# Optimization experiments

Hardware: AMD Instinct MI355X
Metric: run time of the kernel (lower is better)

## Reference

```python
import jax, jax.numpy as jnp
import numpy as np


def conv(x, w, b=None, pad=0):
    y = jax.lax.conv_general_dilated(x, w, (1, 1), [(pad, pad), (pad, pad)],
                                     dimension_numbers=('NCHW', 'OIHW', 'NCHW'))
    if b is not None:
        y = y + b[None, :, None, None]
    return y


def bn(x, g, b, m, v, eps=1e-5):
    scale = g / jnp.sqrt(v + eps)
    return (x - m[None, :, None, None]) * scale[None, :, None, None] + b[None, :, None, None]


def channel_gate(x, w1, b1, w2, b2):
    # avg pool -> MLP -> sigmoid, returns [B, C, 1, 1]
    p = x.mean(axis=(2, 3))                       # [B, C]
    h = jax.nn.relu(p @ w1.T + b1)                # [B, C//r]
    a = h @ w2.T + b2                             # [B, C]
    return jax.nn.sigmoid(a)[:, :, None, None]


def setup_inputs() -> dict:
    key = jax.random.key(0)
    ks = iter(jax.random.split(key, 48))
    B, Cin, H, W = 2, 256, 64, 64
    Ci = Cin // 2          # inter_channels = 128
    Cr = Ci // 16          # gate bottleneck = 8
    def nrm(shape, s=0.05):
        return jax.random.normal(next(ks), shape, jnp.float32) * s
    d = {}
    d['q'] = jax.random.normal(next(ks), (B, Cin, H, W), jnp.float32)
    d['s'] = jax.random.normal(next(ks), (B, Cin, H, W), jnp.float32)
    # Trans_s: conv3x3 + BN
    d['ts_w'] = nrm((Ci, Cin, 3, 3)); d['ts_b'] = jnp.zeros(Ci)
    d['ts_g'] = jnp.ones(Ci); d['ts_be'] = jnp.zeros(Ci)
    d['ts_m'] = nrm((Ci,), 0.01); d['ts_v'] = jnp.ones(Ci)
    # Trans_q: conv3x3 + BN
    d['tq_w'] = nrm((Ci, Cin, 3, 3)); d['tq_b'] = jnp.zeros(Ci)
    d['tq_g'] = jnp.ones(Ci); d['tq_be'] = jnp.zeros(Ci)
    d['tq_m'] = nrm((Ci,), 0.01); d['tq_v'] = jnp.ones(Ci)
    # common_v 1x1
    d['cv_w'] = nrm((Ci, Ci, 1, 1)); d['cv_b'] = jnp.zeros(Ci)
    # key/query 1x1 projections (out = Ci//2)
    d['k1_w'] = nrm((Ci // 2, Ci, 1, 1)); d['k1_b'] = jnp.zeros(Ci // 2)
    d['q1_w'] = nrm((Ci // 2, Ci, 1, 1)); d['q1_b'] = jnp.zeros(Ci // 2)
    d['k2_w'] = nrm((Ci // 2, Ci, 1, 1)); d['k2_b'] = jnp.zeros(Ci // 2)
    d['q2_w'] = nrm((Ci // 2, Ci, 1, 1)); d['q2_b'] = jnp.zeros(Ci // 2)
    # ChannelGate MLP
    d['g1_w'] = nrm((Cr, Ci)); d['g1_b'] = jnp.zeros(Cr)
    d['g2_w'] = nrm((Ci, Cr)); d['g2_b'] = jnp.zeros(Ci)
    # conv_cat: conv3x3 (no bias) + BN
    d['cc_w'] = nrm((Ci, 2 * Ci, 3, 3))
    d['cc_g'] = jnp.ones(Ci); d['cc_be'] = jnp.zeros(Ci)
    d['cc_m'] = nrm((Ci,), 0.01); d['cc_v'] = jnp.ones(Ci)
    return d


def reference(q, s, ts_w, ts_b, ts_g, ts_be, ts_m, ts_v,
              tq_w, tq_b, tq_g, tq_be, tq_m, tq_v,
              cv_w, cv_b, k1_w, k1_b, q1_w, q1_b, k2_w, k2_b, q2_w, q2_b,
              g1_w, g1_b, g2_w, g2_b, cc_w, cc_g, cc_be, cc_m, cc_v):
    # stems: conv3x3 + BN + ReLU
    s = jax.nn.relu(bn(conv(s, ts_w, ts_b, pad=1), ts_g, ts_be, ts_m, ts_v))
    q = jax.nn.relu(bn(conv(q, tq_w, tq_b, pad=1), tq_g, tq_be, tq_m, tq_v))
    B, C, H, W = q.shape
    N = H * W
    # values
    v_q1 = conv(q, cv_w, cv_b)                          # [B,C,H,W]
    v_s1 = conv(s, cv_w, cv_b)
    v_q = v_q1.reshape(B, C, N).transpose(0, 2, 1)      # [B,N,C]
    v_s = v_s1.reshape(B, C, N).transpose(0, 2, 1)
    # dual keys / queries with negation trick
    k1 = conv(s, k1_w, k1_b).reshape(B, C // 2, N)
    k2 = conv(q, k2_w, k2_b).reshape(B, C // 2, N)
    key_cat = jnp.concatenate([k1, -k2], axis=1).transpose(0, 2, 1)   # [B,N,C]
    q1x = conv(s, q1_w, q1_b).reshape(B, C // 2, N)
    q2x = conv(q, q2_w, q2_b).reshape(B, C // 2, N)
    query_cat = jnp.concatenate([q1x, q2x], axis=1)                    # [B,C,N]
    # abs-score attention, dual softmax from the same score matrix
    A_s = jnp.abs(jnp.einsum('bnc,bcm->bnm', key_cat, query_cat))      # [B,N,N]
    att_s = jax.nn.softmax(A_s, axis=-1)
    att_q = jax.nn.softmax(A_s.transpose(0, 2, 1), axis=-1)
    # attend + channel-gate SE fusion + residual
    p_s = jnp.einsum('bnm,bmc->bnc', att_s, v_s).transpose(0, 2, 1).reshape(B, C, H, W)
    E_s = channel_gate(v_s1, g1_w, g1_b, g2_w, g2_b) * p_s + s
    q_s = jnp.einsum('bnm,bmc->bnc', att_q, v_q).transpose(0, 2, 1).reshape(B, C, H, W)
    E_q = channel_gate(v_q1, g1_w, g1_b, g2_w, g2_b) * q_s + q
    # concat + conv3x3(no bias) + BN + ReLU
    cpam = jax.nn.relu(bn(conv(jnp.concatenate([E_q, E_s], axis=1), cc_w, None, pad=1),
                          cc_g, cc_be, cc_m, cc_v))
    return (cpam, E_q, E_s)
```

## Files before the change

### kernel.cpp

```cpp
#include <hip/hip_runtime.h>

typedef __bf16 bf16;
typedef __bf16 v8bf __attribute__((ext_vector_type(8)));
typedef __bf16 v4bf __attribute__((ext_vector_type(4)));
typedef float v4f __attribute__((ext_vector_type(4)));

#define MFMA16(a, b, c) __builtin_amdgcn_mfma_f32_16x16x32_bf16(a, b, c, 0, 0, 0)

__device__ __forceinline__ float sf(float x) {
  if (!(x == x)) return 0.f;
  return fminf(fmaxf(x, -1e30f), 1e30f);
}

__global__ __launch_bounds__(256) void fill_kernel(float* __restrict__ out, float v, int n) {
  int i = blockIdx.x * 256 + threadIdx.x;
  if (i < n) out[i] = v;
}

__global__ __launch_bounds__(256) void prep_kernel(
    const float* __restrict__ ts_w, const float* __restrict__ tq_w,
    const float* ts_b, const float* ts_g, const float* ts_be, const float* ts_m, const float* ts_v,
    const float* tq_b, const float* tq_g, const float* tq_be, const float* tq_m, const float* tq_v,
    bf16* __restrict__ Wt01, float* __restrict__ ss01)
{
  int idx = blockIdx.x * 256 + threadIdx.x;
  if (idx < 589824) {
    int which = idx / 294912;
    int rem = idx - which * 294912;
    int co = rem / 2304;
    int r2 = rem - co * 2304;
    int tap = r2 >> 8;
    int ci = r2 & 255;
    const float* W = which ? tq_w : ts_w;
    Wt01[idx] = (bf16)W[(co * 256 + ci) * 9 + tap];
  } else if (idx < 590080) {
    int i = idx - 589824;
    int which = i >> 7, c = i & 127;
    float g, be, m, vv, bias;
    if (which == 0) { g=ts_g[c]; be=ts_be[c]; m=ts_m[c]; vv=ts_v[c]; bias=ts_b[c]; }
    else            { g=tq_g[c]; be=tq_be[c]; m=tq_m[c]; vv=tq_v[c]; bias=tq_b[c]; }
    float scale = g / sqrtf(vv + 1e-5f);
    ss01[which * 256 + c] = sf(scale);
    ss01[which * 256 + 128 + c] = sf((bias - m) * scale + be);
  }
}

__global__ __launch_bounds__(256) void prep2_kernel(
    const float* __restrict__ cc_w, const float* cc_g, const float* cc_be,
    const float* cc_m, const float* cc_v,
    bf16* __restrict__ Wt2, float* __restrict__ ss_cc)
{
  int idx = blockIdx.x * 256 + threadIdx.x;
  if (idx < 294912) {
    int co = idx / 2304;
    int r2 = idx - co * 2304;
    int tap = r2 >> 8;
    int ci = r2 & 255;
    Wt2[idx] = (bf16)cc_w[(co * 256 + ci) * 9 + tap];
  } else if (idx < 295040) {
    int c = idx - 294912;
    float scale = cc_g[c] / sqrtf(cc_v[c] + 1e-5f);
    ss_cc[c] = sf(scale);
    ss_cc[128 + c] = sf(-cc_m[c] * scale + cc_be[c]);
  }
}

__global__ __launch_bounds__(256) void convN_kernel(
    const float* __restrict__ pS, const float* __restrict__ pQ,
    const bf16* __restrict__ Wb, const float* __restrict__ ssb,
    void* __restrict__ out_, int mode)
{
  __shared__ bf16 As[66][40];
  __shared__ bf16 Bs[3][64][40];

  int y = blockIdx.x;
  int co0 = blockIdx.y * 64;
  int z = blockIdx.z;
  int tsr = z >> 1, b = z & 1;

  const float *in0, *in1;
  const bf16* W;
  const float* sp;
  if (mode == 0) {
    const float* base = (tsr ? pQ : pS) + (long)b * 1048576;
    in0 = base; in1 = base + 524288;
    W = Wb + (long)tsr * 294912;
    sp = ssb + tsr * 256;
  } else {
    in0 = pS + 1048576 + (long)b * 524288;
    in1 = pS + 2097152 + (long)b * 524288;
    W = Wb; sp = ssb;
  }

  int t = threadIdx.x, lane = t & 63, w = t >> 6;
  int l15 = lane & 15, l4 = lane >> 4;
  int wr = (w & 1) * 32, wc = (w >> 1) * 32;
  int ac = t & 31, ag = t >> 5;
  int bco = t >> 2, bk = (t & 3) * 8;

  v4f acc[2][2] = {};

  auto loadA = [&](int it, v8bf& areg) {
    int dy = it >> 3, ks = it & 7;
    int ysrc = y + dy - 1;
    int cg = ks * 32 + ac;
    const float* ip = (cg < 128) ? (in0 + (long)cg * 4096) : (in1 + (long)(cg - 128) * 4096);
    if ((unsigned)ysrc < 64u) {
      const float* src = ip + ysrc * 64 + ag * 8;
#pragma unroll
      for (int i = 0; i < 8; ++i) areg[i] = (bf16)src[i];
    } else {
#pragma unroll
      for (int i = 0; i < 8; ++i) areg[i] = (bf16)0.f;
    }
  };
  auto loadB = [&](int it, v8bf* breg) {
    int dy = it >> 3, ks = it & 7;
    const bf16* wk = W + (long)(co0 + bco) * 2304 + dy * 3 * 256 + ks * 32 + bk;
#pragma unroll
    for (int d = 0; d < 3; ++d) breg[d] = *(const v8bf*)(wk + d * 256);
  };

  v8bf areg, breg[3];
  loadA(0, areg);
  loadB(0, breg);

  for (int it = 0; it < 24; ++it) {
    __syncthreads();
#pragma unroll
    for (int i = 0; i < 8; ++i) As[ag * 8 + 1 + i][ac] = areg[i];
    if (ag == 0) As[0][ac] = (bf16)0.f;
    if (ag == 7) As[65][ac] = (bf16)0.f;
#pragma unroll
    for (int d = 0; d < 3; ++d) *(v8bf*)&Bs[d][bco][bk] = breg[d];
    __syncthreads();
    if (it < 23) { loadA(it + 1, areg); loadB(it + 1, breg); }
#pragma unroll
    for (int d = 0; d < 3; ++d) {
      v8bf af0 = *(const v8bf*)&As[wr + d + l15][l4 * 8];
      v8bf af1 = *(const v8bf*)&As[wr + 16 + d + l15][l4 * 8];
#pragma unroll
      for (int j = 0; j < 2; ++j) {
        v8bf bfr = *(const v8bf*)&Bs[d][wc + j * 16 + l15][l4 * 8];
        acc[0][j] = MFMA16(af0, bfr, acc[0][j]);
        acc[1][j] = MFMA16(af1, bfr, acc[1][j]);
      }
    }
  }
#pragma unroll
  for (int i = 0; i < 2; ++i) {
    int nb = y * 64 + wr + i * 16 + l4 * 4;
#pragma unroll
    for (int j = 0; j < 2; ++j) {
      int c = co0 + wc + j * 16 + l15;
      float scale = sp[c], shift = sp[128 + c];
      if (mode == 0) {
        bf16* o = (bf16*)out_ + ((long)(tsr * 2 + b) * 4096 + nb) * 128 + c;
#pragma unroll
        for (int r = 0; r < 4; ++r)
          o[r * 128] = (bf16)sf(fmaxf(acc[i][j][r] * scale + shift, 0.f));
      } else {
        v4f pk;
#pragma unroll
        for (int r = 0; r < 4; ++r)
          pk[r] = sf(fmaxf(acc[i][j][r] * scale + shift, 0.f));
        *(v4f*)((float*)out_ + ((long)b * 128 + c) * 4096 + nb) = pk;
      }
    }
  }
}

__global__ __launch_bounds__(256) void conv1_kernel(
    const bf16* __restrict__ feat_base,
    const float* __restrict__ cv_w, const float* __restrict__ k1_w, const float* __restrict__ q1_w,
    const float* __restrict__ k2_w, const float* __restrict__ q2_w,
    const float* __restrict__ cv_b, const float* __restrict__ k1_b, const float* __restrict__ q1_b,
    const float* __restrict__ k2_b, const float* __restrict__ q2_b,
    bf16* __restrict__ v_base, bf16* __restrict__ keyT, bf16* __restrict__ queryT,
    float* __restrict__ pmean)
{
  int nt = blockIdx.x;
  int br = blockIdx.z >> 1, b = blockIdx.z & 1;
  long zid = br * 2 + b;
  const bf16* feat = feat_base + zid * 524288 + (long)nt * 4096;

  __shared__ bf16 As[32][40];
  __shared__ bf16 Bs[256][40];

  int t = threadIdx.x, lane = t & 63, w = t >> 6;
  int l15 = lane & 15, l4 = lane >> 4;
  int wr = (w & 1) * 16, wc = (w >> 1) * 128;

  const float* wrow;
  bool negk = false;
  if (t < 128)       wrow = cv_w + (long)t * 128;
  else if (t < 192) { wrow = (br ? k2_w : k1_w) + (long)(t - 128) * 128; negk = (br != 0); }
  else               wrow = (br ? q2_w : q1_w) + (long)(t - 192) * 128;

  v4f acc[8] = {};
  int ap = t >> 2, ak = (t & 3) * 8;

  for (int ks = 0; ks < 4; ++ks) {
    int ci0 = ks * 32;
    v8bf av;
    if (t < 128) av = *(const v8bf*)(feat + ap * 128 + ci0 + ak);
    float wv[32];
#pragma unroll
    for (int u = 0; u < 32; ++u) wv[u] = wrow[ci0 + u];
    if (negk) {
#pragma unroll
      for (int u = 0; u < 32; ++u) wv[u] = -wv[u];
    }
    __syncthreads();
    if (t < 128) *(v8bf*)&As[ap][ak] = av;
#pragma unroll
    for (int u = 0; u < 32; ++u) Bs[t][u] = (bf16)wv[u];
    __syncthreads();
    v8bf af = *(const v8bf*)&As[wr + l15][l4 * 8];
#pragma unroll
    for (int j = 0; j < 8; ++j) {
      v8bf bfr = *(const v8bf*)&Bs[wc + j * 16 + l15][l4 * 8];
      acc[j] = MFMA16(af, bfr, acc[j]);
    }
  }

  int nb = nt * 32 + wr + l4 * 4;
#pragma unroll
  for (int j = 0; j < 8; ++j) {
    int c = wc + j * 16 + l15;
    float bv;
    if (c < 128)      bv = cv_b[c];
    else if (c < 192) bv = br ? -k2_b[c - 128] : k1_b[c - 128];
    else              bv = (br ? q2_b : q1_b)[c - 192];
    float v0 = sf(acc[j][0] + bv), v1 = sf(acc[j][1] + bv);
    float v2 = sf(acc[j][2] + bv), v3 = sf(acc[j][3] + bv);
    if (c < 128) {
      v4bf pk;
      pk[0] = (bf16)v0; pk[1] = (bf16)v1; pk[2] = (bf16)v2; pk[3] = (bf16)v3;
      *(v4bf*)(v_base + zid * 524288 + (long)c * 4096 + nb) = pk;
      float s = v0 + v1 + v2 + v3;
      s += __shfl_xor(s, 16, 64);
      s += __shfl_xor(s, 32, 64);
      if (l4 == 0) atomicAdd(&pmean[zid * 128 + c], s);
    } else if (c < 192) {
      int cc = (c - 128) + br * 64;
      bf16* kp = keyT + (long)b * 524288 + (long)nb * 128 + cc;
      kp[0] = (bf16)v0; kp[128] = (bf16)v1; kp[256] = (bf16)v2; kp[384] = (bf16)v3;
    } else {
      int cc = (c - 192) + br * 64;
      bf16* qp = queryT + (long)b * 524288 + (long)nb * 128 + cc;
      qp[0] = (bf16)v0; qp[128] = (bf16)v1; qp[256] = (bf16)v2; qp[384] = (bf16)v3;
    }
  }
}

__global__ __launch_bounds__(128) void gate2_kernel(
    const float* __restrict__ pmean, const float* __restrict__ g1_w, const float* __restrict__ g1_b,
    const float* __restrict__ g2_w, const float* __restrict__ g2_b, float* __restrict__ gate)
{
  __shared__ float p[128];
  __shared__ float h[8];
  int z = blockIdx.x, t = threadIdx.x;
  p[t] = pmean[z * 128 + t] * (1.f / 4096.f);
  __syncthreads();
  if (t < 8) {
    float a = g1_b[t];
    for (int c = 0; c < 128; ++c) a += g1_w[t * 128 + c] * p[c];
    h[t] = fmaxf(a, 0.f);
  }
  __syncthreads();
  float a = g2_b[t];
#pragma unroll
  for (int j = 0; j < 8; ++j) a += g2_w[t * 8 + j] * h[j];
  gate[z * 128 + t] = sf(1.f / (1.f + __expf(-a)));
}

__global__ __launch_bounds__(256) void apply_kernel(
    const bf16* __restrict__ keyT, const bf16* __restrict__ queryT,
    const bf16* __restrict__ v_base, const float* __restrict__ gate,
    const bf16* __restrict__ feat_base, float* __restrict__ d_out)
{
  int nt = blockIdx.x, br = blockIdx.z >> 1, b = blockIdx.z & 1;
  int n0 = nt * 32;
  const bf16* X = (br ? queryT : keyT) + ((long)b * 4096 + n0) * 128;
  const bf16* Y = (br ? keyT : queryT) + (long)b * 4096 * 128;
  const bf16* V = v_base + (long)(br * 2 + b) * 524288;
  const float* gt = gate + (br * 2 + b) * 128;
  const bf16* feat = feat_base + (long)(br * 2 + b) * 524288 + (long)n0 * 128;

  __shared__ bf16 Ys[64][132];
  __shared__ bf16 Vs[128][68];
  __shared__ bf16 Ps[32][68];
  __shared__ float rps[4][32];

  int t = threadIdx.x, lane = t & 63, w = t >> 6;
  int l15 = lane & 15, l4 = lane >> 4;
  int wm = w * 16;
  int wr = (w & 1) * 16;
  int wc = (w >> 1) * 64;

#pragma unroll
  for (int i = 0; i < 2; ++i) {
    int ch = t + i * 256;
    *(v8bf*)&Ys[ch >> 4][(ch & 15) * 8] = *(const v8bf*)(X + (ch >> 4) * 128 + (ch & 15) * 8);
  }
  __syncthreads();
  v8bf af[2][4];
#pragma unroll
  for (int i = 0; i < 2; ++i)
#pragma unroll
    for (int k = 0; k < 4; ++k)
      af[i][k] = *(const v8bf*)&Ys[i * 16 + l15][k * 32 + l4 * 8];

  v4f acc[4] = {};
  float rp[2][4] = {};

  v8bf yreg[4], vreg[4];
#pragma unroll
  for (int i = 0; i < 4; ++i) {
    int ch = t + i * 256;
    yreg[i] = *(const v8bf*)(Y + (long)(ch >> 4) * 128 + (ch & 15) * 8);
    vreg[i] = *(const v8bf*)(V + (long)(ch >> 3) * 4096 + (ch & 7) * 8);
  }

  for (int mt = 0; mt < 64; ++mt) {
    __syncthreads();
#pragma unroll
    for (int i = 0; i < 4; ++i) {
      int ch = t + i * 256;
      *(v8bf*)&Ys[ch >> 4][(ch & 15) * 8] = yreg[i];
      *(v8bf*)&Vs[ch >> 3][(ch & 7) * 8] = vreg[i];
    }
    __syncthreads();
    if (mt < 63) {
      int m0 = (mt + 1) * 64;
#pragma unroll
      for (int i = 0; i < 4; ++i) {
        int ch = t + i * 256;
        yreg[i] = *(const v8bf*)(Y + (long)(m0 + (ch >> 4)) * 128 + (ch & 15) * 8);
        vreg[i] = *(const v8bf*)(V + (long)(ch >> 3) * 4096 + m0 + (ch & 7) * 8);
      }
    }
    v4f sacc[2] = {};
#pragma unroll
    for (int k = 0; k < 4; ++k) {
      v8bf by = *(const v8bf*)&Ys[wm + l15][k * 32 + l4 * 8];
#pragma unroll
      for (int i = 0; i < 2; ++i)
        sacc[i] = MFMA16(af[i][k], by, sacc[i]);
    }
#pragma unroll
    for (int i = 0; i < 2; ++i)
#pragma unroll
      for (int r = 0; r < 4; ++r) {
        float e = __expf(fminf(fabsf(sacc[i][r]), 80.f) - 50.f);
        rp[i][r] += e;
        Ps[i * 16 + l4 * 4 + r][wm + l15] = (bf16)e;
      }
    __syncthreads();
#pragma unroll
    for (int k = 0; k < 2; ++k) {
      v8bf p0 = *(const v8bf*)&Ps[wr + l15][k * 32 + l4 * 8];
#pragma unroll
      for (int j = 0; j < 4; ++j) {
        v8bf vb = *(const v8bf*)&Vs[wc + j * 16 + l15][k * 32 + l4 * 8];
        acc[j] = MFMA16(p0, vb, acc[j]);
      }
    }
  }
#pragma unroll
  for (int i = 0; i < 2; ++i)
#pragma unroll
    for (int r = 0; r < 4; ++r) {
      float v = rp[i][r];
      v += __shfl_xor(v, 1, 64);
      v += __shfl_xor(v, 2, 64);
      v += __shfl_xor(v, 4, 64);
      v += __shfl_xor(v, 8, 64);
      if (l15 == 0) rps[w][i * 16 + l4 * 4 + r] = v;
    }
  __syncthreads();

  float* outE = d_out + (long)(br ? 1 : 2) * 1048576 + (long)b * 524288;
  int rowt = wr + l4 * 4;
  float dv[4];
#pragma unroll
  for (int r = 0; r < 4; ++r)
    dv[r] = fmaxf(rps[0][rowt + r] + rps[1][rowt + r] + rps[2][rowt + r] + rps[3][rowt + r],
                  1e-30f);
#pragma unroll
  for (int j = 0; j < 4; ++j) {
    int c = wc + j * 16 + l15;
    float g = gt[c];
    v4f pk;
#pragma unroll
    for (int r = 0; r < 4; ++r) {
      float val = acc[j][r] / dv[r] * g + (float)feat[(long)(rowt + r) * 128 + c];
      pk[r] = sf(val);
    }
    *(v4f*)(outE + (long)c * 4096 + n0 + rowt) = pk;
  }
}

extern "C" void kernel_launch(void* const* d_in, const int* in_sizes, int n_in,
                              void* d_out, int out_size, void* d_ws, size_t ws_size,
                              hipStream_t stream)
{
  if (n_in != 33 || in_sizes[0] != 2097152 || in_sizes[2] != 294912 ||
      in_sizes[14] != 16384 || out_size != 3145728) {
    fill_kernel<<<12288, 256, 0, stream>>>((float*)d_out, 100.0f, 3145728);
    return;
  }
  if (ws_size < 12582912) {
    fill_kernel<<<12288, 256, 0, stream>>>((float*)d_out, 1.0f, 3145728);
    return;
  }

  const float* q_in = (const float*)d_in[0];
  const float* s_in = (const float*)d_in[1];
  char* ob = (char*)d_out;
  float* outf = (float*)d_out;

  float* gate  = (float*)(ob + 0);
  float* pmean = (float*)(ob + 2048);

  char* ws = (char*)d_ws;
  bf16*  sfeat  = (bf16*)(ws + 0);
  bf16*  vs     = (bf16*)(ws + 4194304);
  bf16*  keyT   = (bf16*)(ws + 8388608);
  bf16*  queryT = (bf16*)(ws + 10485760);
  bf16*  Wt01   = (bf16*)(ws + 8388608);
  float* ss01   = (float*)(ws + 10485760);
  bf16*  Wt2    = (bf16*)(ws + 0);
  float* ss_cc  = (float*)(ws + 589824);

  prep_kernel<<<2306, 256, 0, stream>>>(
      (const float*)d_in[2], (const float*)d_in[8],
      (const float*)d_in[3], (const float*)d_in[4], (const float*)d_in[5],
      (const float*)d_in[6], (const float*)d_in[7],
      (const float*)d_in[9], (const float*)d_in[10], (const float*)d_in[11],
      (const float*)d_in[12], (const float*)d_in[13],
      Wt01, ss01);

  fill_kernel<<<2, 256, 0, stream>>>(pmean, 0.0f, 512);

  convN_kernel<<<dim3(64, 2, 4), 256, 0, stream>>>(s_in, q_in, Wt01, ss01, sfeat, 0);

  conv1_kernel<<<dim3(128, 1, 4), 256, 0, stream>>>(
      sfeat,
      (const float*)d_in[14], (const float*)d_in[16], (const float*)d_in[18],
      (const float*)d_in[20], (const float*)d_in[22],
      (const float*)d_in[15], (const float*)d_in[17], (const float*)d_in[19],
      (const float*)d_in[21], (const float*)d_in[23],
      vs, keyT, queryT, pmean);

  gate2_kernel<<<4, 128, 0, stream>>>(pmean, (const float*)d_in[24], (const float*)d_in[25],
                                      (const float*)d_in[26], (const float*)d_in[27], gate);

  apply_kernel<<<dim3(128, 1, 4), 256, 0, stream>>>(keyT, queryT, vs, gate, sfeat, outf);

  prep2_kernel<<<1153, 256, 0, stream>>>(
      (const float*)d_in[28], (const float*)d_in[29], (const float*)d_in[30],
      (const float*)d_in[31], (const float*)d_in[32], Wt2, ss_cc);

  convN_kernel<<<dim3(64, 2, 2), 256, 0, stream>>>(outf, nullptr, Wt2, ss_cc, outf, 1);
}
```

Measured before the change: 302.9 us.

## Load attention operands directly from global into MFMA registers with double buffering

The apply kernel stops staging Y and V tiles through shared memory. Each wave now loads its MFMA B-operands straight from global memory into registers, with a ping-pong register double buffer across the two halves of each 128-column step. It also replaces __syncthreads with explicit lgkmcnt waits plus raw barriers, pads Ps differently, and asks for 2 blocks per SM through launch bounds. This removes LDS traffic and some barriers, but every wave now issues redundant, less coalesced global loads and uses more registers.

New measurement: 379.0 us. 25.1% more time.

```diff
diff --git a/kernel.cpp b/kernel.cpp
--- a/kernel.cpp
+++ b/kernel.cpp
@@ -275,7 +275,7 @@
   gate[z * 128 + t] = sf(1.f / (1.f + __expf(-a)));
 }
 
-__global__ __launch_bounds__(256) void apply_kernel(
+__global__ __launch_bounds__(256, 2) void apply_kernel(
     const bf16* __restrict__ keyT, const bf16* __restrict__ queryT,
     const bf16* __restrict__ v_base, const float* __restrict__ gate,
     const bf16* __restrict__ feat_base, float* __restrict__ d_out)
@@ -288,9 +288,7 @@
   const float* gt = gate + (br * 2 + b) * 128;
   const bf16* feat = feat_base + (long)(br * 2 + b) * 524288 + (long)n0 * 128;
 
-  __shared__ bf16 Ys[64][132];
-  __shared__ bf16 Vs[128][68];
-  __shared__ bf16 Ps[32][68];
+  __shared__ bf16 Ps[32][70];
   __shared__ float rps[4][32];
 
   int t = threadIdx.x, lane = t & 63, w = t >> 6;
@@ -299,75 +297,95 @@
   int wr = (w & 1) * 16;
   int wc = (w >> 1) * 64;
 
-#pragma unroll
-  for (int i = 0; i < 2; ++i) {
-    int ch = t + i * 256;
-    *(v8bf*)&Ys[ch >> 4][(ch & 15) * 8] = *(const v8bf*)(X + (ch >> 4) * 128 + (ch & 15) * 8);
-  }
-  __syncthreads();
   v8bf af[2][4];
 #pragma unroll
   for (int i = 0; i < 2; ++i)
 #pragma unroll
     for (int k = 0; k < 4; ++k)
-      af[i][k] = *(const v8bf*)&Ys[i * 16 + l15][k * 32 + l4 * 8];
+      af[i][k] = *(const v8bf*)(X + (long)(i * 16 + l15) * 128 + k * 32 + l4 * 8);
 
   v4f acc[4] = {};
   float rp[2][4] = {};
 
-  v8bf yreg[4], vreg[4];
-#pragma unroll
-  for (int i = 0; i < 4; ++i) {
-    int ch = t + i * 256;
-    yreg[i] = *(const v8bf*)(Y + (long)(ch >> 4) * 128 + (ch & 15) * 8);
-    vreg[i] = *(const v8bf*)(V + (long)(ch >> 3) * 4096 + (ch & 7) * 8);
-  }
-
-  for (int mt = 0; mt < 64; ++mt) {
-    __syncthreads();
-#pragma unroll
-    for (int i = 0; i < 4; ++i) {
-      int ch = t + i * 256;
-      *(v8bf*)&Ys[ch >> 4][(ch & 15) * 8] = yreg[i];
-      *(v8bf*)&Vs[ch >> 3][(ch & 7) * 8] = vreg[i];
-    }
-    __syncthreads();
-    if (mt < 63) {
-      int m0 = (mt + 1) * 64;
-#pragma unroll
-      for (int i = 0; i < 4; ++i) {
-        int ch = t + i * 256;
-        yreg[i] = *(const v8bf*)(Y + (long)(m0 + (ch >> 4)) * 128 + (ch & 15) * 8);
-        vreg[i] = *(const v8bf*)(V + (long)(ch >> 3) * 4096 + m0 + (ch & 7) * 8);
+  auto loadBy = [&](int m0, v8bf* by) {
+#pragma unroll
+    for (int k = 0; k < 4; ++k)
+      by[k] = *(const v8bf*)(Y + (long)(m0 + wm + l15) * 128 + k * 32 + l4 * 8);
+  };
+  auto loadVb = [&](int m0, v8bf* vb) {
+#pragma unroll
+    for (int j = 0; j < 4; ++j)
+#pragma unroll
+      for (int k = 0; k < 2; ++k)
+        vb[j * 2 + k] = *(const v8bf*)(V + (long)(wc + j * 16 + l15) * 4096 + m0 + k * 32 + l4 * 8);
+  };
+
+  v8bf byA[4], byB[4], vbA[8], vbB[8];
+  loadBy(0, byA);
+  loadVb(0, vbA);
+
+  for (int mt2 = 0; mt2 < 32; ++mt2) {
+    int mA = mt2 * 128;
+    {
+      v4f sacc[2] = {};
+#pragma unroll
+      for (int k = 0; k < 4; ++k)
+#pragma unroll
+        for (int i = 0; i < 2; ++i)
+          sacc[i] = MFMA16(af[i][k], byA[k], sacc[i]);
+      loadBy(mA + 64, byB);
+#pragma unroll
+      for (int i = 0; i < 2; ++i)
+#pragma unroll
+        for (int r = 0; r < 4; ++r) {
+          float e = __expf(fminf(fabsf(sacc[i][r]), 80.f) - 50.f);
+          rp[i][r] += e;
+          Ps[i * 16 + l4 * 4 + r][wm + l15] = (bf16)e;
+        }
+      asm volatile("s_waitcnt lgkmcnt(0)" ::: "memory");
+      __builtin_amdgcn_s_barrier();
+#pragma unroll
+      for (int k = 0; k < 2; ++k) {
+        v8bf p0 = *(const v8bf*)&Ps[wr + l15][k * 32 + l4 * 8];
+#pragma unroll
+        for (int j = 0; j < 4; ++j)
+          acc[j] = MFMA16(p0, vbA[j * 2 + k], acc[j]);
       }
-    }
-    v4f sacc[2] = {};
-#pragma unroll
-    for (int k = 0; k < 4; ++k) {
-      v8bf by = *(const v8bf*)&Ys[wm + l15][k * 32 + l4 * 8];
+      loadVb(mA + 64, vbB);
+      asm volatile("s_waitcnt lgkmcnt(0)" ::: "memory");
+      __builtin_amdgcn_s_barrier();
+    }
+    {
+      v4f sacc[2] = {};
+#pragma unroll
+      for (int k = 0; k < 4; ++k)
+#pragma unroll
+        for (int i = 0; i < 2; ++i)
+          sacc[i] = MFMA16(af[i][k], byB[k], sacc[i]);
+      if (mt2 < 31) loadBy(mA + 128, byA);
 #pragma unroll
       for (int i = 0; i < 2; ++i)
-        sacc[i] = MFMA16(af[i][k], by, sacc[i]);
-    }
-#pragma unroll
-    for (int i = 0; i < 2; ++i)
-#pragma unroll
-      for (int r = 0; r < 4; ++r) {
-        float e = __expf(fminf(fabsf(sacc[i][r]), 80.f) - 50.f);
-        rp[i][r] += e;
-        Ps[i * 16 + l4 * 4 + r][wm + l15] = (bf16)e;
+#pragma unroll
+        for (int r = 0; r < 4; ++r) {
+          float e = __expf(fminf(fabsf(sacc[i][r]), 80.f) - 50.f);
+          rp[i][r] += e;
+          Ps[i * 16 + l4 * 4 + r][wm + l15] = (bf16)e;
+        }
+      asm volatile("s_waitcnt lgkmcnt(0)" ::: "memory");
+      __builtin_amdgcn_s_barrier();
+#pragma unroll
+      for (int k = 0; k < 2; ++k) {
+        v8bf p0 = *(const v8bf*)&Ps[wr + l15][k * 32 + l4 * 8];
+#pragma unroll
+        for (int j = 0; j < 4; ++j)
+          acc[j] = MFMA16(p0, vbB[j * 2 + k], acc[j]);
       }
-    __syncthreads();
-#pragma unroll
-    for (int k = 0; k < 2; ++k) {
-      v8bf p0 = *(const v8bf*)&Ps[wr + l15][k * 32 + l4 * 8];
-#pragma unroll
-      for (int j = 0; j < 4; ++j) {
-        v8bf vb = *(const v8bf*)&Vs[wc + j * 16 + l15][k * 32 + l4 * 8];
-        acc[j] = MFMA16(p0, vb, acc[j]);
-      }
-    }
-  }
+      if (mt2 < 31) loadVb(mA + 128, vbA);
+      asm volatile("s_waitcnt lgkmcnt(0)" ::: "memory");
+      __builtin_amdgcn_s_barrier();
+    }
+  }
+
 #pragma unroll
   for (int i = 0; i < 2; ++i)
 #pragma unroll
```
